# Performance work log

Hardware: AMD Instinct MI355X
Metric: run time of the kernel (lower is better)

Reference implementation:

```python
import jax, jax.numpy as jnp
import numpy as np
from jax import lax

N = 512      # num_nodes in the graph
FEAT = 128   # args.feat_dim (node tag vocab)
EMB = 64     # embedding_size (input_feat width = 2*EMB = 128, per node_order.repeat(1,128))
HID = 128    # args.hidden / LSTM hidden size
NMLP = 4


def setup_inputs() -> dict:
    key = jax.random.key(0)
    ks = jax.random.split(key, 12)
    s = 0.05
    return {
        "node_tags": jax.random.randint(ks[0], (N,), 0, FEAT),
        "adj": jax.random.uniform(ks[1], (N, N), dtype=jnp.float32),
        "label": jax.random.randint(ks[2], (1,), 0, 2),
        "W_emb": jax.random.normal(ks[3], (FEAT, EMB), jnp.float32) * s,
        "b_emb": jnp.zeros((EMB,), jnp.float32),
        "W_ih": jax.random.normal(ks[4], (4 * HID, 2 * EMB), jnp.float32) * s,
        "W_hh": jax.random.normal(ks[5], (4 * HID, HID), jnp.float32) * s,
        "b_ih": jnp.zeros((4 * HID,), jnp.float32),
        "b_hh": jnp.zeros((4 * HID,), jnp.float32),
        "W1s": jax.random.normal(ks[6], (NMLP, HID, HID), jnp.float32) * s,
        "b1s": jnp.zeros((NMLP, HID), jnp.float32),
        "W2s": jax.random.normal(ks[7], (NMLP, HID), jnp.float32) * s,
        "b2s": jnp.zeros((NMLP,), jnp.float32),
        "var_raw": jax.random.normal(ks[8], (NMLP,), jnp.float32) * s,
    }


def _node_orders(adj, key):
    """Greedy noisy random-walk ordering from every start node. [N,N] int32."""
    n = adj.shape[0]
    starts = jnp.arange(n)
    keys = jax.random.split(key, n)

    def one_start(start, k):
        mask0 = jnp.ones((n,), jnp.float32).at[start].set(0.0)

        def step(carry, t):
            cur, mask = carry
            noise = jax.random.uniform(jax.random.fold_in(k, t), (n,),
                                       minval=0.01, maxval=0.1)
            prob = jnp.exp(jnp.take(adj, cur, axis=0) + noise)
            prob = (prob / prob.sum()) * mask  # masked: visited -> 0
            nxt = jnp.argmax(prob)
            return (nxt, mask.at[nxt].set(0.0)), nxt

        _, rest = lax.scan(step, (start, mask0), jnp.arange(n - 1))
        return jnp.concatenate([start[None], rest])

    return jax.vmap(one_start)(starts, keys)


def _lstm(x, W_ih, W_hh, b_ih, b_hh):
    # x: [T, B, In] -> out [T, B, H]
    T, B, _ = x.shape
    H = W_hh.shape[1]
    b = b_ih + b_hh

    def step(carry, xt):
        h, c = carry
        gates = xt @ W_ih.T + h @ W_hh.T + b           # [B, 4H]
        i, f, g, o = jnp.split(gates, 4, axis=-1)      # torch gate order i,f,g,o
        c = jax.nn.sigmoid(f) * c + jax.nn.sigmoid(i) * jnp.tanh(g)
        h = jax.nn.sigmoid(o) * jnp.tanh(c)
        return (h, c), h

    h0 = jnp.zeros((B, H), x.dtype)
    _, out = lax.scan(step, (h0, h0), x)
    return out


def reference(node_tags, adj, label, W_emb, b_emb, W_ih, W_hh, b_ih, b_hh,
              W1s, b1s, W2s, b2s, var_raw):
    n = adj.shape[0]
    onehot = jax.nn.one_hot(node_tags, W_emb.shape[0], dtype=jnp.float32)
    node_feat = onehot @ W_emb + b_emb                       # [N, EMB]
    A = (adj > 0.5).astype(jnp.float32)                      # binary adjacency
    neigh_feat = (A @ onehot) @ W_emb + b_emb                # neighbor tag histogram -> embed
    input_feat = jnp.concatenate([node_feat, neigh_feat], 1) # [N, 2*EMB]

    orders = _node_orders(adj, jax.random.key(42))           # [Nstart, Nstep]
    batch = input_feat[orders]                               # [Nstart, Nstep, 2E]
    batch = jnp.transpose(batch, (1, 0, 2))                  # [T=N, B=N, 2E]

    out = _lstm(batch, W_ih, W_hh, b_ih, b_hh)               # [T, B, HID]
    embed = out.mean(axis=0)                                 # [N, HID]

    # 4-way ensemble MLP heads (batched over k)
    h = jax.nn.relu(jnp.einsum('nd,kdh->knh', embed, W1s) + b1s[:, None, :])
    logits = jnp.einsum('knh,kh->kn', h, W2s) + b2s[:, None] # [4, N]
    y = jax.nn.sigmoid(logits)
    lab = label[0].astype(jnp.float32)
    bce = -(lab * jax.nn.log_sigmoid(logits)
            + (1.0 - lab) * jax.nn.log_sigmoid(-logits)).mean(axis=1)  # [4]
    loss_ = bce.sum()

    var_w = jax.nn.softplus(var_raw)                         # per-head weight
    c = var_w / var_w.sum()
    y_ = (c[:, None] * y).sum(axis=0)                        # [N]
    return loss_, y_
```

## Files before the change

kernel.cpp:

```cpp
#include <hip/hip_runtime.h>
#include <hip/hip_bf16.h>
#include <stdint.h>

#define NN 512
#define FEAT 128
#define EMBD 64
#define HID 128

typedef float f32x4 __attribute__((ext_vector_type(4)));
typedef short s16x8 __attribute__((ext_vector_type(8)));

__device__ __forceinline__ uint32_t rotl32(uint32_t v, int s){ return (v << s) | (v >> (32 - s)); }

__device__ __forceinline__ void tf2x32(uint32_t k0, uint32_t k1, uint32_t x0, uint32_t x1,
                                       uint32_t &o0, uint32_t &o1){
  uint32_t k2 = k0 ^ k1 ^ 0x1BD11BDAu;
  x0 += k0; x1 += k1;
  x0+=x1; x1=rotl32(x1,13); x1^=x0;
  x0+=x1; x1=rotl32(x1,15); x1^=x0;
  x0+=x1; x1=rotl32(x1,26); x1^=x0;
  x0+=x1; x1=rotl32(x1, 6); x1^=x0;
  x0 += k1; x1 += k2 + 1u;
  x0+=x1; x1=rotl32(x1,17); x1^=x0;
  x0+=x1; x1=rotl32(x1,29); x1^=x0;
  x0+=x1; x1=rotl32(x1,16); x1^=x0;
  x0+=x1; x1=rotl32(x1,24); x1^=x0;
  x0 += k2; x1 += k0 + 2u;
  x0+=x1; x1=rotl32(x1,13); x1^=x0;
  x0+=x1; x1=rotl32(x1,15); x1^=x0;
  x0+=x1; x1=rotl32(x1,26); x1^=x0;
  x0+=x1; x1=rotl32(x1, 6); x1^=x0;
  x0 += k0; x1 += k1 + 3u;
  x0+=x1; x1=rotl32(x1,17); x1^=x0;
  x0+=x1; x1=rotl32(x1,29); x1^=x0;
  x0+=x1; x1=rotl32(x1,16); x1^=x0;
  x0+=x1; x1=rotl32(x1,24); x1^=x0;
  x0 += k1; x1 += k2 + 4u;
  x0+=x1; x1=rotl32(x1,13); x1^=x0;
  x0+=x1; x1=rotl32(x1,15); x1^=x0;
  x0+=x1; x1=rotl32(x1,26); x1^=x0;
  x0+=x1; x1=rotl32(x1, 6); x1^=x0;
  x0 += k2; x1 += k0 + 5u;
  o0 = x0; o1 = x1;
}

__device__ __forceinline__ float bits_to_noise(uint32_t bits){
  float u = __builtin_bit_cast(float, (bits >> 9) | 0x3f800000u) - 1.0f;
  const float dlt = 0.1f - 0.01f;
  float v = __fadd_rn(__fmul_rn(u, dlt), 0.01f);
  return fmaxf(0.01f, v);
}

__device__ __forceinline__ short f2bf(float f){
  uint32_t u = __builtin_bit_cast(uint32_t, f);
  u += 0x7fffu + ((u >> 16) & 1u);
  return (short)(u >> 16);
}

__device__ __forceinline__ float fsig(float x){
  return __builtin_amdgcn_rcpf(1.0f + __expf(-x));
}
__device__ __forceinline__ float ftanh(float x){
  float e = __expf(2.0f * x);
  return 1.0f - 2.0f * __builtin_amdgcn_rcpf(e + 1.0f);
}
__device__ __forceinline__ float softplusf(float x){
  return log1pf(expf(x));
}

__device__ __forceinline__ void lds_barrier(){
  asm volatile("s_waitcnt lgkmcnt(0)\n\ts_barrier" ::: "memory");
}

__device__ __forceinline__ float wave_fmax(float x){
  int xi;
  #define DSTEP(C) xi = __builtin_amdgcn_update_dpp(0, __builtin_bit_cast(int,x), C, 0xF, 0xF, true); \
                   x = fmaxf(x, __builtin_bit_cast(float,xi));
  DSTEP(0xB1)
  DSTEP(0x4E)
  DSTEP(0x141)
  DSTEP(0x140)
  #undef DSTEP
  xi = __builtin_amdgcn_ds_swizzle(__builtin_bit_cast(int,x), 0x401F);
  x = fmaxf(x, __builtin_bit_cast(float,xi));
  x = fmaxf(x, __shfl_xor(x, 32));
  return x;
}
__device__ __forceinline__ uint32_t wave_maxu(uint32_t x){
  int m;
  #define USTEP(C) m = __builtin_amdgcn_update_dpp(0, (int)x, C, 0xF, 0xF, true); \
                   x = x > (uint32_t)m ? x : (uint32_t)m;
  USTEP(0xB1) USTEP(0x4E) USTEP(0x141) USTEP(0x140)
  #undef USTEP
  m = __builtin_amdgcn_ds_swizzle((int)x, 0x401F);
  x = x > (uint32_t)m ? x : (uint32_t)m;
  uint32_t o = (uint32_t)__shfl_xor((int)x, 32);
  x = x > o ? x : o;
  return x;
}

__device__ __forceinline__ void orders_body(const float* __restrict__ adj,
                                            int* __restrict__ orders, int s){
  int lane = threadIdx.x;
  __shared__ uint32_t kts[2*(NN-1)];
  __shared__ float ca[NN];
  __shared__ int   ci[NN];

  uint32_t ks0, ks1; tf2x32(0u, 42u, 0u, (uint32_t)s, ks0, ks1);
  for (int t = lane; t < NN-1; t += 64){
    uint32_t a, b; tf2x32(ks0, ks1, 0u, (uint32_t)t, a, b);
    kts[2*t] = a; kts[2*t+1] = b;
  }
  __syncthreads();

  uint32_t vis = 0;
  if ((s >> 3) == lane) vis |= 1u << (s & 7);
  int cur = s;
  if (lane == 0) orders[(size_t)s*NN] = s;
  unsigned long long lt = (1ull << lane) - 1ull;

  for (int t = 0; t < NN-1; ++t){
    uint32_t kt0 = kts[2*t], kt1 = kts[2*t+1];
    const float4* r4 = (const float4*)(adj + (size_t)cur*NN);
    float4 v0 = r4[lane*2], v1 = r4[lane*2+1];
    float a[8] = {v0.x,v0.y,v0.z,v0.w,v1.x,v1.y,v1.z,v1.w};

    float mx = -1.f;
    #pragma unroll
    for (int e = 0; e < 8; ++e)
      mx = fmaxf(mx, ((vis >> e) & 1) ? -1.f : a[e]);
    mx = wave_fmax(mx);
    float T = mx - 0.0901f;

    int base = 0, pos[8]; uint32_t cm = 0;
    #pragma unroll
    for (int e = 0; e < 8; ++e){
      bool c = !((vis >> e) & 1) && (a[e] >= T);
      unsigned long long bal = __ballot(c);
      pos[e] = base + __popcll(bal & lt);
      base += __popcll(bal);
      if (c) cm |= 1u << e;
    }
    #pragma unroll
    for (int e = 0; e < 8; ++e)
      if ((cm >> e) & 1){ ca[pos[e]] = a[e]; ci[pos[e]] = lane*8 + e; }
    int total = base;

    uint32_t bk = 0; int bi = 0x7fffffff;
    for (int b0 = 0; b0 < total; b0 += 64){
      int k = b0 + lane;
      if (k < total){
        int idx = ci[k]; float av = ca[k];
        uint32_t x0, x1;
        tf2x32(kt0, kt1, 0u, (uint32_t)idx, x0, x1);
        float nz = bits_to_noise(x0 ^ x1);
        uint32_t a23 = (uint32_t)(av * 8388608.0f);
        uint32_t n30 = (uint32_t)(nz * 1073741824.0f);
        uint32_t key = (a23 << 7) + n30;
        if (key > bk || (key == bk && idx < bi)){ bk = key; bi = idx; }
      }
    }
    uint32_t km = wave_maxu(bk);
    unsigned long long msk = __ballot(bk == km);
    int widx;
    if (__popcll(msk) == 1){
      widx = __shfl(bi, __ffsll((long long)msk) - 1);
    } else {
      int iv = (bk == km) ? bi : 0x7fffffff;
      #pragma unroll
      for (int off = 1; off < 64; off <<= 1){
        int o = __shfl_xor(iv, off);
        iv = o < iv ? o : iv;
      }
      widx = iv;
    }
    cur = widx;
    if ((widx >> 3) == lane) vis |= 1u << (widx & 7);
    if (lane == 0) orders[(size_t)s*NN + t + 1] = widx;
  }
}

__device__ __forceinline__ void featifw_body(int n, const int* __restrict__ tags,
    const float* __restrict__ adj, const float* __restrict__ W_emb,
    const float* __restrict__ b_emb, const float* __restrict__ W_ih,
    const float* __restrict__ b_ih, const float* __restrict__ b_hh,
    float* __restrict__ IFW){
  int tid = threadIdx.x;
  __shared__ int tg[NN];
  __shared__ __align__(16) float xs[2*EMBD];
  for (int i = tid; i < NN; i += 64) tg[i] = tags[i];
  float nf = W_emb[tg[n]*EMBD + tid] + b_emb[tid];
  float ac = 0.f;
  for (int m = 0; m < NN; ++m){
    if (adj[(size_t)n*NN + m] > 0.5f) ac += W_emb[tg[m]*EMBD + tid];
  }
  xs[tid]        = nf;
  xs[EMBD + tid] = ac + b_emb[tid];
  __syncthreads();
  const float4* xs4 = (const float4*)xs;
  for (int it = 0; it < 8; ++it){
    int g = it*64 + tid;
    const float4* wr4 = (const float4*)(W_ih + (size_t)g*(2*EMBD));
    float a2 = b_ih[g] + b_hh[g];
    #pragma unroll 8
    for (int kk = 0; kk < 32; ++kk){
      float4 wv = wr4[kk], xv = xs4[kk];
      a2 += wv.x*xv.x + wv.y*xv.y + wv.z*xv.z + wv.w*xv.w;
    }
    IFW[(size_t)n*(4*HID) + (g & 127)*4 + (g >> 7)] = a2;
  }
}

__global__ __launch_bounds__(64) void k_mega1(const float* __restrict__ adj,
    int* __restrict__ orders, const int* __restrict__ tags,
    const float* __restrict__ W_emb, const float* __restrict__ b_emb,
    const float* __restrict__ W_ih, const float* __restrict__ b_ih,
    const float* __restrict__ b_hh, float* __restrict__ IFW){
  if (blockIdx.x < NN) orders_body(adj, orders, blockIdx.x);
  else                 featifw_body(blockIdx.x - NN, tags, adj, W_emb, b_emb,
                                    W_ih, b_ih, b_hh, IFW);
}

__device__ __forceinline__ void lstm_step(int t, int w, int l15, int l4,
    const short (*hread)[HID+8], short (*hwrite)[HID+8],
    f32x4 (&vC)[4], f32x4 (&vN)[4],
    const s16x8 (&Bf)[4][4], float (&c)[4], float (&emb)[4],
    const int* ord_s, const float* __restrict__ IFW2){
  int tn = (t + 1 < NN) ? t + 1 : NN - 1;
  #pragma unroll
  for (int r = 0; r < 4; ++r){
    int ord = ord_s[(l4*4 + r)*NN + tn];
    vN[r] = *(const f32x4*)(IFW2 + (size_t)ord*(4*HID) + (w*16 + l15)*4);
  }
  s16x8 Af[4];
  #pragma unroll
  for (int kt = 0; kt < 4; ++kt)
    Af[kt] = *(const s16x8*)&hread[l15][kt*32 + l4*8];
  f32x4 acc[4];
  #pragma unroll
  for (int q = 0; q < 4; ++q){
    f32x4 a = {vC[0][q], vC[1][q], vC[2][q], vC[3][q]};
    #pragma unroll
    for (int kt = 0; kt < 4; ++kt)
      a = __builtin_amdgcn_mfma_f32_16x16x32_bf16(Af[kt], Bf[q][kt], a, 0, 0, 0);
    acc[q] = a;
  }
  int col = w*16 + l15;
  #pragma unroll
  for (int r = 0; r < 4; ++r){
    float si = fsig(acc[0][r]);
    float sf = fsig(acc[1][r]);
    float tg = ftanh(acc[2][r]);
    float so = fsig(acc[3][r]);
    float cn = sf * c[r] + si * tg;
    c[r] = cn;
    float h = so * ftanh(cn);
    emb[r] += h;
    hwrite[l4*4 + r][col] = f2bf(h);
  }
  lds_barrier();
}

__global__ __launch_bounds__(512, 2) void k_lstm(const float* __restrict__ W_hh,
    const float* __restrict__ IFW2, const int* __restrict__ orders,
    const float* __restrict__ W1s, const float* __restrict__ b1s,
    const float* __restrict__ W2s, const float* __restrict__ b2s,
    float* __restrict__ logits){
  int wg = blockIdx.x, tid = threadIdx.x;
  int w = tid >> 6, l = tid & 63, l15 = l & 15, l4 = l >> 4;
  __shared__ int ord_s[16*NN];
  __shared__ __align__(16) short hbuf[2][16][HID+8];
  __shared__ float part[4][2];

  for (int i = tid; i < 16*NN; i += 512){
    int m = i >> 9, t = i & (NN-1);
    ord_s[i] = orders[(size_t)(16*wg + m)*NN + t];
  }
  for (int i = tid; i < 16*(HID+8); i += 512)
    ((short*)hbuf[0])[i] = 0;

  s16x8 Bf[4][4];
  #pragma unroll
  for (int q = 0; q < 4; ++q)
    #pragma unroll
    for (int kt = 0; kt < 4; ++kt){
      int g = q*HID + w*16 + l15;
      const float* src = W_hh + (size_t)g*HID + kt*32 + l4*8;
      s16x8 v;
      #pragma unroll
      for (int e = 0; e < 8; ++e) v[e] = f2bf(src[e]);
      Bf[q][kt] = v;
    }
  __syncthreads();

  float c[4] = {0,0,0,0}, emb[4] = {0,0,0,0};
  f32x4 vA[4], vB[4];
  #pragma unroll
  for (int r = 0; r < 4; ++r){
    int ord = ord_s[(l4*4 + r)*NN];
    vA[r] = *(const f32x4*)(IFW2 + (size_t)ord*(4*HID) + (w*16 + l15)*4);
  }

  for (int t2 = 0; t2 < NN/2; ++t2){
    lstm_step(2*t2,     w, l15, l4, hbuf[0], hbuf[1], vA, vB, Bf, c, emb, ord_s, IFW2);
    lstm_step(2*t2 + 1, w, l15, l4, hbuf[1], hbuf[0], vB, vA, Bf, c, emb, ord_s, IFW2);
  }

  float* eL = (float*)&hbuf[0][0][0];
  #pragma unroll
  for (int r = 0; r < 4; ++r)
    eL[(l4*4 + r)*HID + w*16 + l15] = emb[r] * (1.0f/512.0f);
  __syncthreads();

  int hk = tid >> 7;
  int u  = tid & 127;
  float b1v = b1s[hk*HID + u];
  float w2v = W2s[hk*HID + u];
  const float* wcol = W1s + (size_t)hk*HID*HID + u;
  for (int m = 0; m < 16; ++m){
    const float4* es4 = (const float4*)(eL + m*HID);
    float pre = b1v;
    #pragma unroll 4
    for (int d4 = 0; d4 < 32; ++d4){
      float4 e4 = es4[d4];
      pre += e4.x * wcol[(4*d4+0)*HID];
      pre += e4.y * wcol[(4*d4+1)*HID];
      pre += e4.z * wcol[(4*d4+2)*HID];
      pre += e4.w * wcol[(4*d4+3)*HID];
    }
    float v = fmaxf(pre, 0.f) * w2v;
    #pragma unroll
    for (int off = 1; off < 64; off <<= 1) v += __shfl_xor(v, off);
    if (l == 0) part[hk][(tid >> 6) & 1] = v;
    __syncthreads();
    if (tid < 4) logits[tid*NN + 16*wg + m] = part[tid][0] + part[tid][1] + b2s[tid];
    __syncthreads();
  }
}

__global__ __launch_bounds__(512) void k_final(const float* __restrict__ logits,
                                               const int* __restrict__ label,
                                               const float* __restrict__ var_raw,
                                               float* __restrict__ out){
  int n = threadIdx.x;
  float lab = (float)label[0];
  float sp[4]; float tot = 0.f;
  #pragma unroll
  for (int k = 0; k < 4; ++k){ sp[k] = softplusf(var_raw[k]); tot += sp[k]; }
  float y = 0.f, bce = 0.f;
  #pragma unroll
  for (int k = 0; k < 4; ++k){
    float x = logits[k*NN + n];
    float yk = 1.0f / (1.0f + expf(-x));
    y += (sp[k] / tot) * yk;
    bce += lab * softplusf(-x) + (1.0f - lab) * softplusf(x);
  }
  out[1 + n] = y;
  __shared__ float pr[8];
  #pragma unroll
  for (int off = 1; off < 64; off <<= 1) bce += __shfl_xor(bce, off);
  if ((n & 63) == 0) pr[n >> 6] = bce;
  __syncthreads();
  if (n == 0){
    float ssum = 0.f;
    for (int i = 0; i < 8; ++i) ssum += pr[i];
    out[0] = ssum * (1.0f/512.0f);
  }
}

extern "C" void kernel_launch(void* const* d_in, const int* in_sizes, int n_in,
                              void* d_out, int out_size, void* d_ws, size_t ws_size,
                              hipStream_t stream) {
  const int*   node_tags = (const int*)  d_in[0];
  const float* adj       = (const float*)d_in[1];
  const int*   label     = (const int*)  d_in[2];
  const float* W_emb     = (const float*)d_in[3];
  const float* b_emb     = (const float*)d_in[4];
  const float* W_ih      = (const float*)d_in[5];
  const float* W_hh      = (const float*)d_in[6];
  const float* b_ih      = (const float*)d_in[7];
  const float* b_hh      = (const float*)d_in[8];
  const float* W1s       = (const float*)d_in[9];
  const float* b1s       = (const float*)d_in[10];
  const float* W2s       = (const float*)d_in[11];
  const float* b2s       = (const float*)d_in[12];
  const float* var_raw   = (const float*)d_in[13];
  float* out = (float*)d_out;

  float* ws     = (float*)d_ws;
  float* IFW    = ws + 65536;
  float* logits = IFW + 262144 + 65536;
  int*   orders = (int*)(logits + 2048);

  k_mega1<<<dim3(2*NN), dim3(64), 0, stream>>>(adj, orders, node_tags, W_emb,
                                               b_emb, W_ih, b_ih, b_hh, IFW);
  k_lstm <<<dim3(32),  dim3(512), 0, stream>>>(W_hh, IFW, orders, W1s, b1s,
                                               W2s, b2s, logits);
  k_final<<<dim3(1),   dim3(512), 0, stream>>>(logits, label, var_raw, out);
}
```

Measured before the change: 1.127 ms.

## Spread LSTM over 128 blocks of 4 sequences and prefetch next adj row

The LSTM kernel now handles 4 sequences per 512-thread block instead of 16, launching 128 blocks rather than 32 so more CUs take part in the serial 512-step recurrence. MFMA results go through a shared-memory gate buffer so that every thread applies the pointwise gates to one hidden unit, at the cost of two barriers per step and mostly wasted MFMA rows. The orders walk packs the adjacency value and index into one 32-bit shared word, and it issues the next row's adjacency load right after the argmax so the load starts earlier.

Result: faster. 1.103 ms (-2.1%).

```diff
diff --git a/kernel.cpp b/kernel.cpp
--- a/kernel.cpp
+++ b/kernel.cpp
@@ -103,8 +103,7 @@
                                             int* __restrict__ orders, int s){
   int lane = threadIdx.x;
   __shared__ uint32_t kts[2*(NN-1)];
-  __shared__ float ca[NN];
-  __shared__ int   ci[NN];
+  __shared__ uint32_t pcs[NN];
 
   uint32_t ks0, ks1; tf2x32(0u, 42u, 0u, (uint32_t)s, ks0, ks1);
   for (int t = lane; t < NN-1; t += 64){
@@ -115,14 +114,14 @@
 
   uint32_t vis = 0;
   if ((s >> 3) == lane) vis |= 1u << (s & 7);
-  int cur = s;
   if (lane == 0) orders[(size_t)s*NN] = s;
   unsigned long long lt = (1ull << lane) - 1ull;
 
+  const float4* r4 = (const float4*)(adj + (size_t)s*NN);
+  float4 v0 = r4[lane*2], v1 = r4[lane*2+1];
+
   for (int t = 0; t < NN-1; ++t){
     uint32_t kt0 = kts[2*t], kt1 = kts[2*t+1];
-    const float4* r4 = (const float4*)(adj + (size_t)cur*NN);
-    float4 v0 = r4[lane*2], v1 = r4[lane*2+1];
     float a[8] = {v0.x,v0.y,v0.z,v0.w,v1.x,v1.y,v1.z,v1.w};
 
     float mx = -1.f;
@@ -143,20 +142,23 @@
     }
     #pragma unroll
     for (int e = 0; e < 8; ++e)
-      if ((cm >> e) & 1){ ca[pos[e]] = a[e]; ci[pos[e]] = lane*8 + e; }
+      if ((cm >> e) & 1){
+        uint32_t a23 = (uint32_t)(a[e] * 8388608.0f);
+        pcs[pos[e]] = (a23 << 9) | (uint32_t)(lane*8 + e);
+      }
     int total = base;
 
     uint32_t bk = 0; int bi = 0x7fffffff;
     for (int b0 = 0; b0 < total; b0 += 64){
       int k = b0 + lane;
       if (k < total){
-        int idx = ci[k]; float av = ca[k];
+        uint32_t pc = pcs[k];
+        int idx = (int)(pc & 511u);
         uint32_t x0, x1;
         tf2x32(kt0, kt1, 0u, (uint32_t)idx, x0, x1);
         float nz = bits_to_noise(x0 ^ x1);
-        uint32_t a23 = (uint32_t)(av * 8388608.0f);
         uint32_t n30 = (uint32_t)(nz * 1073741824.0f);
-        uint32_t key = (a23 << 7) + n30;
+        uint32_t key = ((pc >> 9) << 7) + n30;
         if (key > bk || (key == bk && idx < bi)){ bk = key; bi = idx; }
       }
     }
@@ -174,7 +176,8 @@
       }
       widx = iv;
     }
-    cur = widx;
+    const float4* nr = (const float4*)(adj + (size_t)widx*NN);
+    v0 = nr[lane*2]; v1 = nr[lane*2+1];
     if ((widx >> 3) == lane) vis |= 1u << (widx & 7);
     if (lane == 0) orders[(size_t)s*NN + t + 1] = widx;
   }
@@ -221,46 +224,6 @@
                                     W_ih, b_ih, b_hh, IFW);
 }
 
-__device__ __forceinline__ void lstm_step(int t, int w, int l15, int l4,
-    const short (*hread)[HID+8], short (*hwrite)[HID+8],
-    f32x4 (&vC)[4], f32x4 (&vN)[4],
-    const s16x8 (&Bf)[4][4], float (&c)[4], float (&emb)[4],
-    const int* ord_s, const float* __restrict__ IFW2){
-  int tn = (t + 1 < NN) ? t + 1 : NN - 1;
-  #pragma unroll
-  for (int r = 0; r < 4; ++r){
-    int ord = ord_s[(l4*4 + r)*NN + tn];
-    vN[r] = *(const f32x4*)(IFW2 + (size_t)ord*(4*HID) + (w*16 + l15)*4);
-  }
-  s16x8 Af[4];
-  #pragma unroll
-  for (int kt = 0; kt < 4; ++kt)
-    Af[kt] = *(const s16x8*)&hread[l15][kt*32 + l4*8];
-  f32x4 acc[4];
-  #pragma unroll
-  for (int q = 0; q < 4; ++q){
-    f32x4 a = {vC[0][q], vC[1][q], vC[2][q], vC[3][q]};
-    #pragma unroll
-    for (int kt = 0; kt < 4; ++kt)
-      a = __builtin_amdgcn_mfma_f32_16x16x32_bf16(Af[kt], Bf[q][kt], a, 0, 0, 0);
-    acc[q] = a;
-  }
-  int col = w*16 + l15;
-  #pragma unroll
-  for (int r = 0; r < 4; ++r){
-    float si = fsig(acc[0][r]);
-    float sf = fsig(acc[1][r]);
-    float tg = ftanh(acc[2][r]);
-    float so = fsig(acc[3][r]);
-    float cn = sf * c[r] + si * tg;
-    c[r] = cn;
-    float h = so * ftanh(cn);
-    emb[r] += h;
-    hwrite[l4*4 + r][col] = f2bf(h);
-  }
-  lds_barrier();
-}
-
 __global__ __launch_bounds__(512, 2) void k_lstm(const float* __restrict__ W_hh,
     const float* __restrict__ IFW2, const int* __restrict__ orders,
     const float* __restrict__ W1s, const float* __restrict__ b1s,
@@ -268,16 +231,17 @@
     float* __restrict__ logits){
   int wg = blockIdx.x, tid = threadIdx.x;
   int w = tid >> 6, l = tid & 63, l15 = l & 15, l4 = l >> 4;
-  __shared__ int ord_s[16*NN];
-  __shared__ __align__(16) short hbuf[2][16][HID+8];
+  int em = tid >> 7, eu = tid & 127;
+
+  __shared__ int ord_s[4*NN];
+  __shared__ __align__(16) short hbuf[16][HID+8];
+  __shared__ __align__(16) float gl[4][520];
   __shared__ float part[4][2];
 
-  for (int i = tid; i < 16*NN; i += 512){
-    int m = i >> 9, t = i & (NN-1);
-    ord_s[i] = orders[(size_t)(16*wg + m)*NN + t];
-  }
+  for (int i = tid; i < 4*NN; i += 512)
+    ord_s[i] = orders[(size_t)(4*wg)*NN + i];
   for (int i = tid; i < 16*(HID+8); i += 512)
-    ((short*)hbuf[0])[i] = 0;
+    ((short*)hbuf)[i] = 0;
 
   s16x8 Bf[4][4];
   #pragma unroll
@@ -293,31 +257,71 @@
     }
   __syncthreads();
 
-  float c[4] = {0,0,0,0}, emb[4] = {0,0,0,0};
-  f32x4 vA[4], vB[4];
-  #pragma unroll
-  for (int r = 0; r < 4; ++r){
-    int ord = ord_s[(l4*4 + r)*NN];
-    vA[r] = *(const f32x4*)(IFW2 + (size_t)ord*(4*HID) + (w*16 + l15)*4);
-  }
-
-  for (int t2 = 0; t2 < NN/2; ++t2){
-    lstm_step(2*t2,     w, l15, l4, hbuf[0], hbuf[1], vA, vB, Bf, c, emb, ord_s, IFW2);
-    lstm_step(2*t2 + 1, w, l15, l4, hbuf[1], hbuf[0], vB, vA, Bf, c, emb, ord_s, IFW2);
-  }
-
-  float* eL = (float*)&hbuf[0][0][0];
-  #pragma unroll
-  for (int r = 0; r < 4; ++r)
-    eL[(l4*4 + r)*HID + w*16 + l15] = emb[r] * (1.0f/512.0f);
+  int u = w*16 + l15;
+  float cst = 0.f, emb = 0.f;
+
+  f32x4 vif[4];
+  if (l4 == 0){
+    #pragma unroll
+    for (int r = 0; r < 4; ++r)
+      vif[r] = *(const f32x4*)(IFW2 + (size_t)ord_s[r*NN]*(4*HID) + u*4);
+  }
+
+  for (int t = 0; t < NN; ++t){
+    s16x8 Af[4];
+    #pragma unroll
+    for (int kt = 0; kt < 4; ++kt)
+      Af[kt] = *(const s16x8*)&hbuf[l15][kt*32 + l4*8];
+
+    f32x4 acc[4];
+    #pragma unroll
+    for (int q = 0; q < 4; ++q){
+      f32x4 a = {0.f, 0.f, 0.f, 0.f};
+      #pragma unroll
+      for (int kt = 0; kt < 4; ++kt)
+        a = __builtin_amdgcn_mfma_f32_16x16x32_bf16(Af[kt], Bf[q][kt], a, 0, 0, 0);
+      acc[q] = a;
+    }
+
+    int tn = (t + 1 < NN) ? t + 1 : NN - 1;
+    f32x4 vifn[4];
+    if (l4 == 0){
+      #pragma unroll
+      for (int r = 0; r < 4; ++r)
+        vifn[r] = *(const f32x4*)(IFW2 + (size_t)ord_s[r*NN + tn]*(4*HID) + u*4);
+      #pragma unroll
+      for (int q = 0; q < 4; ++q)
+        #pragma unroll
+        for (int r = 0; r < 4; ++r)
+          gl[r][u*4 + q] = acc[q][r] + vif[r][q];
+    }
+    lds_barrier();
+
+    f32x4 g4 = *(const f32x4*)&gl[em][eu*4];
+    float si = fsig(g4[0]);
+    float sf = fsig(g4[1]);
+    float tg = ftanh(g4[2]);
+    float so = fsig(g4[3]);
+    float cn = sf * cst + si * tg;
+    cst = cn;
+    float h = so * ftanh(cn);
+    emb += h;
+    hbuf[em][eu] = f2bf(h);
+    #pragma unroll
+    for (int r = 0; r < 4; ++r) vif[r] = vifn[r];
+    lds_barrier();
+  }
+
+  float* eL = (float*)gl;
+  eL[em*HID + eu] = emb * (1.0f/512.0f);
   __syncthreads();
 
   int hk = tid >> 7;
-  int u  = tid & 127;
-  float b1v = b1s[hk*HID + u];
-  float w2v = W2s[hk*HID + u];
-  const float* wcol = W1s + (size_t)hk*HID*HID + u;
-  for (int m = 0; m < 16; ++m){
+  int uu = tid & 127;
+  float b1v = b1s[hk*HID + uu];
+  float w2v = W2s[hk*HID + uu];
+  const float* wcol = W1s + (size_t)hk*HID*HID + uu;
+  for (int m = 0; m < 4; ++m){
     const float4* es4 = (const float4*)(eL + m*HID);
     float pre = b1v;
     #pragma unroll 4
@@ -333,7 +337,7 @@
     for (int off = 1; off < 64; off <<= 1) v += __shfl_xor(v, off);
     if (l == 0) part[hk][(tid >> 6) & 1] = v;
     __syncthreads();
-    if (tid < 4) logits[tid*NN + 16*wg + m] = part[tid][0] + part[tid][1] + b2s[tid];
+    if (tid < 4) logits[tid*NN + 4*wg + m] = part[tid][0] + part[tid][1] + b2s[tid];
     __syncthreads();
   }
 }
@@ -394,7 +398,7 @@
 
   k_mega1<<<dim3(2*NN), dim3(64), 0, stream>>>(adj, orders, node_tags, W_emb,
                                                b_emb, W_ih, b_ih, b_hh, IFW);
-  k_lstm <<<dim3(32),  dim3(512), 0, stream>>>(W_hh, IFW, orders, W1s, b1s,
+  k_lstm <<<dim3(128), dim3(512), 0, stream>>>(W_hh, IFW, orders, W1s, b1s,
                                                W2s, b2s, logits);
   k_final<<<dim3(1),   dim3(512), 0, stream>>>(logits, label, var_raw, out);
 }
```

## Split LSTM across 128 workgroups of 4 sequences with transposed MFMA

Applied to the files above, without the earlier changes.

The LSTM kernel now runs 128 workgroups of 256 threads, each handling 4 sequences, instead of 32 workgroups handling 16. The MFMA is transposed so W_hh is the A operand and the hidden state is B. Gate results go through an LDS buffer, and each thread finishes two hidden units with an extra barrier per step. The aim is to occupy more CUs on the 512-step serial recurrence and cut per-step latency. In exchange, most of the MFMA output is wasted (only 4 of 16 columns are used), and each step pays an extra LDS round trip and barrier.

After: 1.090 ms. 1.03x faster.

```diff
diff --git a/kernel.cpp b/kernel.cpp
--- a/kernel.cpp
+++ b/kernel.cpp
@@ -8,6 +8,7 @@
 #define HID 128
 
 typedef float f32x4 __attribute__((ext_vector_type(4)));
+typedef short s16x4 __attribute__((ext_vector_type(4)));
 typedef short s16x8 __attribute__((ext_vector_type(8)));
 
 __device__ __forceinline__ uint32_t rotl32(uint32_t v, int s){ return (v << s) | (v >> (32 - s)); }
@@ -221,120 +222,149 @@
                                     W_ih, b_ih, b_hh, IFW);
 }
 
-__device__ __forceinline__ void lstm_step(int t, int w, int l15, int l4,
-    const short (*hread)[HID+8], short (*hwrite)[HID+8],
-    f32x4 (&vC)[4], f32x4 (&vN)[4],
-    const s16x8 (&Bf)[4][4], float (&c)[4], float (&emb)[4],
-    const int* ord_s, const float* __restrict__ IFW2){
-  int tn = (t + 1 < NN) ? t + 1 : NN - 1;
-  #pragma unroll
-  for (int r = 0; r < 4; ++r){
-    int ord = ord_s[(l4*4 + r)*NN + tn];
-    vN[r] = *(const f32x4*)(IFW2 + (size_t)ord*(4*HID) + (w*16 + l15)*4);
-  }
-  s16x8 Af[4];
-  #pragma unroll
-  for (int kt = 0; kt < 4; ++kt)
-    Af[kt] = *(const s16x8*)&hread[l15][kt*32 + l4*8];
-  f32x4 acc[4];
-  #pragma unroll
-  for (int q = 0; q < 4; ++q){
-    f32x4 a = {vC[0][q], vC[1][q], vC[2][q], vC[3][q]};
-    #pragma unroll
-    for (int kt = 0; kt < 4; ++kt)
-      a = __builtin_amdgcn_mfma_f32_16x16x32_bf16(Af[kt], Bf[q][kt], a, 0, 0, 0);
-    acc[q] = a;
-  }
-  int col = w*16 + l15;
-  #pragma unroll
-  for (int r = 0; r < 4; ++r){
-    float si = fsig(acc[0][r]);
-    float sf = fsig(acc[1][r]);
-    float tg = ftanh(acc[2][r]);
-    float so = fsig(acc[3][r]);
-    float cn = sf * c[r] + si * tg;
-    c[r] = cn;
-    float h = so * ftanh(cn);
-    emb[r] += h;
-    hwrite[l4*4 + r][col] = f2bf(h);
-  }
-  lds_barrier();
-}
-
-__global__ __launch_bounds__(512, 2) void k_lstm(const float* __restrict__ W_hh,
+__global__ __launch_bounds__(256, 1) void k_lstm(const float* __restrict__ W_hh,
     const float* __restrict__ IFW2, const int* __restrict__ orders,
     const float* __restrict__ W1s, const float* __restrict__ b1s,
     const float* __restrict__ W2s, const float* __restrict__ b2s,
     float* __restrict__ logits){
   int wg = blockIdx.x, tid = threadIdx.x;
   int w = tid >> 6, l = tid & 63, l15 = l & 15, l4 = l >> 4;
-  __shared__ int ord_s[16*NN];
-  __shared__ __align__(16) short hbuf[2][16][HID+8];
+  int es = tid >> 6, u = tid & 63;
+
+  __shared__ int ord_s[4*NN];
+  __shared__ __align__(16) short hbuf[2][4][HID+8];
+  __shared__ __align__(16) float gl[4*512];
   __shared__ float part[4][2];
 
-  for (int i = tid; i < 16*NN; i += 512){
-    int m = i >> 9, t = i & (NN-1);
-    ord_s[i] = orders[(size_t)(16*wg + m)*NN + t];
-  }
-  for (int i = tid; i < 16*(HID+8); i += 512)
-    ((short*)hbuf[0])[i] = 0;
-
-  s16x8 Bf[4][4];
+  for (int i = tid; i < 4*NN; i += 256)
+    ord_s[i] = orders[(size_t)(4*wg + (i >> 9))*NN + (i & 511)];
+  for (int i = tid; i < 2*4*(HID+8); i += 256)
+    ((short*)hbuf)[i] = 0;
+
+  s16x8 Wf[4][2][4];
   #pragma unroll
   for (int q = 0; q < 4; ++q)
     #pragma unroll
-    for (int kt = 0; kt < 4; ++kt){
-      int g = q*HID + w*16 + l15;
-      const float* src = W_hh + (size_t)g*HID + kt*32 + l4*8;
-      s16x8 v;
+    for (int j = 0; j < 2; ++j)
       #pragma unroll
-      for (int e = 0; e < 8; ++e) v[e] = f2bf(src[e]);
-      Bf[q][kt] = v;
-    }
-  __syncthreads();
-
-  float c[4] = {0,0,0,0}, emb[4] = {0,0,0,0};
-  f32x4 vA[4], vB[4];
-  #pragma unroll
-  for (int r = 0; r < 4; ++r){
-    int ord = ord_s[(l4*4 + r)*NN];
-    vA[r] = *(const f32x4*)(IFW2 + (size_t)ord*(4*HID) + (w*16 + l15)*4);
-  }
-
-  for (int t2 = 0; t2 < NN/2; ++t2){
-    lstm_step(2*t2,     w, l15, l4, hbuf[0], hbuf[1], vA, vB, Bf, c, emb, ord_s, IFW2);
-    lstm_step(2*t2 + 1, w, l15, l4, hbuf[1], hbuf[0], vB, vA, Bf, c, emb, ord_s, IFW2);
-  }
-
-  float* eL = (float*)&hbuf[0][0][0];
-  #pragma unroll
-  for (int r = 0; r < 4; ++r)
-    eL[(l4*4 + r)*HID + w*16 + l15] = emb[r] * (1.0f/512.0f);
-  __syncthreads();
-
-  int hk = tid >> 7;
-  int u  = tid & 127;
-  float b1v = b1s[hk*HID + u];
-  float w2v = W2s[hk*HID + u];
-  const float* wcol = W1s + (size_t)hk*HID*HID + u;
-  for (int m = 0; m < 16; ++m){
-    const float4* es4 = (const float4*)(eL + m*HID);
-    float pre = b1v;
-    #pragma unroll 4
-    for (int d4 = 0; d4 < 32; ++d4){
-      float4 e4 = es4[d4];
-      pre += e4.x * wcol[(4*d4+0)*HID];
-      pre += e4.y * wcol[(4*d4+1)*HID];
-      pre += e4.z * wcol[(4*d4+2)*HID];
-      pre += e4.w * wcol[(4*d4+3)*HID];
-    }
-    float v = fmaxf(pre, 0.f) * w2v;
-    #pragma unroll
-    for (int off = 1; off < 64; off <<= 1) v += __shfl_xor(v, off);
-    if (l == 0) part[hk][(tid >> 6) & 1] = v;
-    __syncthreads();
-    if (tid < 4) logits[tid*NN + 16*wg + m] = part[tid][0] + part[tid][1] + b2s[tid];
-    __syncthreads();
+      for (int kt = 0; kt < 4; ++kt){
+        int g = q*HID + w*32 + j*16 + l15;
+        const float* src = W_hh + (size_t)g*HID + kt*32 + l4*8;
+        s16x8 v;
+        #pragma unroll
+        for (int e = 0; e < 8; ++e) v[e] = f2bf(src[e]);
+        Wf[q][j][kt] = v;
+      }
+  __syncthreads();
+
+  float c0 = 0.f, c1 = 0.f, emb0 = 0.f, emb1 = 0.f;
+
+  f32x4 vifA, vifB, vifnA, vifnB;
+  {
+    int ord = ord_s[es*NN];
+    const float* b = IFW2 + (size_t)ord*(4*HID);
+    vifA = *(const f32x4*)(b + u*4);
+    vifB = *(const f32x4*)(b + (u+64)*4);
+  }
+
+  for (int t = 0; t < NN; ++t){
+    int pb = t & 1, wb = 1 - pb;
+
+    int tn = (t + 1 < NN) ? t + 1 : NN - 1;
+    {
+      int ord = ord_s[es*NN + tn];
+      const float* b = IFW2 + (size_t)ord*(4*HID);
+      vifnA = *(const f32x4*)(b + u*4);
+      vifnB = *(const f32x4*)(b + (u+64)*4);
+    }
+
+    s16x8 Hf[4];
+    #pragma unroll
+    for (int kt = 0; kt < 4; ++kt)
+      Hf[kt] = *(const s16x8*)&hbuf[pb][l15 & 3][kt*32 + l4*8];
+
+    f32x4 acc[4][2];
+    #pragma unroll
+    for (int q = 0; q < 4; ++q)
+      #pragma unroll
+      for (int j = 0; j < 2; ++j){
+        f32x4 a = {0.f, 0.f, 0.f, 0.f};
+        #pragma unroll
+        for (int kt = 0; kt < 4; ++kt)
+          a = __builtin_amdgcn_mfma_f32_16x16x32_bf16(Wf[q][j][kt], Hf[kt], a, 0, 0, 0);
+        acc[q][j] = a;
+      }
+
+    if (l15 < 4){
+      #pragma unroll
+      for (int q = 0; q < 4; ++q)
+        #pragma unroll
+        for (int j = 0; j < 2; ++j)
+          *(f32x4*)&gl[l15*512 + q*128 + w*32 + j*16 + l4*4] = acc[q][j];
+    }
+    lds_barrier();
+
+    {
+      float gi = gl[es*512 +       u] + vifA[0];
+      float gf = gl[es*512 + 128 + u] + vifA[1];
+      float gg = gl[es*512 + 256 + u] + vifA[2];
+      float go = gl[es*512 + 384 + u] + vifA[3];
+      float cn = fsig(gf) * c0 + fsig(gi) * ftanh(gg);
+      c0 = cn;
+      float h = fsig(go) * ftanh(cn);
+      emb0 += h;
+      hbuf[wb][es][u] = f2bf(h);
+    }
+    {
+      int u2 = u + 64;
+      float gi = gl[es*512 +       u2] + vifB[0];
+      float gf = gl[es*512 + 128 + u2] + vifB[1];
+      float gg = gl[es*512 + 256 + u2] + vifB[2];
+      float go = gl[es*512 + 384 + u2] + vifB[3];
+      float cn = fsig(gf) * c1 + fsig(gi) * ftanh(gg);
+      c1 = cn;
+      float h = fsig(go) * ftanh(cn);
+      emb1 += h;
+      hbuf[wb][es][u2] = f2bf(h);
+    }
+    vifA = vifnA; vifB = vifnB;
+    lds_barrier();
+  }
+
+  __syncthreads();
+  float* eL = gl;
+  eL[es*HID + u]      = emb0 * (1.0f/512.0f);
+  eL[es*HID + u + 64] = emb1 * (1.0f/512.0f);
+  __syncthreads();
+
+  int uu = tid & 127, kk = tid >> 7;
+  for (int k2 = 0; k2 < 2; ++k2){
+    int k = kk*2 + k2;
+    float b1v = b1s[k*HID + uu];
+    float w2v = W2s[k*HID + uu];
+    const float* wcol = W1s + (size_t)k*HID*HID + uu;
+    for (int m = 0; m < 4; ++m){
+      const float4* es4 = (const float4*)(eL + m*HID);
+      float pre = b1v;
+      #pragma unroll 4
+      for (int d4 = 0; d4 < 32; ++d4){
+        float4 e4 = es4[d4];
+        pre += e4.x * wcol[(4*d4+0)*HID];
+        pre += e4.y * wcol[(4*d4+1)*HID];
+        pre += e4.z * wcol[(4*d4+2)*HID];
+        pre += e4.w * wcol[(4*d4+3)*HID];
+      }
+      float v = fmaxf(pre, 0.f) * w2v;
+      #pragma unroll
+      for (int off = 1; off < 64; off <<= 1) v += __shfl_xor(v, off);
+      if (l == 0) part[k][(tid >> 6) & 1] = v;
+      __syncthreads();
+      if (tid < 2){
+        int ko = tid*2 + k2;
+        logits[ko*NN + 4*wg + m] = part[ko][0] + part[ko][1] + b2s[ko];
+      }
+      __syncthreads();
+    }
   }
 }
 
@@ -394,7 +424,7 @@
 
   k_mega1<<<dim3(2*NN), dim3(64), 0, stream>>>(adj, orders, node_tags, W_emb,
                                                b_emb, W_ih, b_ih, b_hh, IFW);
-  k_lstm <<<dim3(32),  dim3(512), 0, stream>>>(W_hh, IFW, orders, W1s, b1s,
+  k_lstm <<<dim3(128), dim3(256), 0, stream>>>(W_hh, IFW, orders, W1s, b1s,
                                                W2s, b2s, logits);
   k_final<<<dim3(1),   dim3(512), 0, stream>>>(logits, label, var_raw, out);
 }
```
